# Performance work log

Measured on AMD Instinct MI355X. Metric: run time of the kernel, lower is better.

The kernel has to match this reference:

```python
import jax, jax.numpy as jnp
import numpy as np

B, S, H, E, TOPK = 2, 2048, 1024, 8, 2
CAP_FACTOR = 1.5
CAPACITY = int(B * S * CAP_FACTOR * TOPK / E)  # 1536


def setup_inputs() -> dict:
    key = jax.random.key(0)
    k1, k2, k3 = jax.random.split(key, 3)
    s = 1.0 / np.sqrt(H)
    return {
        "hidden_states": jax.random.normal(k1, (B, S, H), jnp.float32),
        "W1": jax.random.normal(k2, (H, H), jnp.float32) * s,
        "b1": jnp.zeros((H,), jnp.float32),
        "W2": jax.random.normal(k3, (H, E), jnp.float32) * s,
        "b2": jnp.zeros((E,), jnp.float32),
    }


def reference(hidden_states, W1, b1, W2, b2):
    # Router MLP: Linear -> ReLU -> Linear
    h = jax.nn.relu(jnp.einsum("bsh,hk->bsk", hidden_states, W1) + b1)
    logits = jnp.einsum("bsh,he->bse", h, W2) + b2          # [B,S,E]
    probs = jax.nn.softmax(logits, axis=-1)                   # [B,S,E]

    topk_p, topk_i = jax.lax.top_k(probs, TOPK)               # [B,S,K]
    topk_p = topk_p / jnp.sum(topk_p, axis=-1, keepdims=True)

    N = B * S
    idx = topk_i.reshape(N, TOPK)                             # [N,K] int
    p = topk_p.reshape(N, TOPK)                               # [N,K]
    pos = jnp.arange(N)

    dispatch = jnp.zeros((N, E, CAPACITY), jnp.float32)
    combine = jnp.zeros((N, E, CAPACITY), jnp.float32)
    # Faithful to torch semantics: expert_count[idx] += 1 uses non-accumulating
    # index_put, so duplicates within one top-k slot collapse to a single +1.
    count = jnp.zeros((E,), jnp.int32)
    for i in range(TOPK):  # small fixed loop over top-k slots
        e = idx[:, i]                  # [N]
        pr = p[:, i]                   # [N]
        c_e = count[e]                 # slot position for each token's expert
        ok = c_e < CAPACITY
        # (pos, e, c_e) triples are unique per token; prior value is always 0,
        # so masked-out tokens just rewrite 0.
        dispatch = dispatch.at[pos, e, c_e].set(jnp.where(ok, 1.0, 0.0))
        combine = combine.at[pos, e, c_e].set(jnp.where(ok, pr, 0.0))
        # within a slot all tokens of expert e write the same value -> deterministic
        count = count.at[e].set(jnp.where(ok, c_e + 1, c_e))

    dispatch = dispatch.reshape(B, S, E, CAPACITY)
    combine = combine.reshape(B, S, E, CAPACITY)

    per_expert = probs.mean(axis=(0, 1))                      # [E]
    aux_loss = jnp.sum(per_expert * jnp.log(per_expert * E + 1e-9))
    return dispatch, combine, probs, aux_loss
```

## Files before the change

### kernel.cpp

```cpp
#include <hip/hip_runtime.h>

#define TOKENS 4096
#define HDIM   1024
#define EDIM   8
#define CAP    1536

typedef float f32x4 __attribute__((ext_vector_type(4)));

#define BM 128
#define BN 64
#define BK 16
#define ZF4_PER_BLOCK 49152

__global__ __launch_bounds__(256, 2) void gemm1_relu_fill(
    const float* __restrict__ X, const float* __restrict__ W1,
    const float* __restrict__ b1, float* __restrict__ Hout,
    float* __restrict__ zreg, int* __restrict__ flags)
{
    __shared__ float As[BK][BM + 4];
    __shared__ float Bs[BK][BN];
    const int K = HDIM, N = HDIM;
    const int tid  = threadIdx.x;
    const int arow = tid >> 1;
    const int acol = (tid & 1) << 3;
    const int brow = tid >> 4;
    const int bcol = (tid & 15) << 2;
    const int tx   = tid & 15;
    const int ty   = tid >> 4;

    const float* Ab = X  + (size_t)(blockIdx.y * BM) * K;
    const float* Bb = W1 + blockIdx.x * BN;

    const int blk = blockIdx.y * gridDim.x + blockIdx.x;
    if (blk == 0 && tid < EDIM) flags[tid] = 0;
    f32x4* Z = (f32x4*)zreg + (size_t)blk * ZF4_PER_BLOCK + tid;
    const f32x4 z4 = {0.f, 0.f, 0.f, 0.f};

    float acc[8][4] = {};
    int zs = 0;
    for (int k0 = 0; k0 < K; k0 += BK) {
        float4 a0 = *(const float4*)(Ab + (size_t)arow * K + k0 + acol);
        float4 a1 = *(const float4*)(Ab + (size_t)arow * K + k0 + acol + 4);
        float4 bv = *(const float4*)(Bb + (size_t)(k0 + brow) * N + bcol);
        As[acol + 0][arow] = a0.x;
        As[acol + 1][arow] = a0.y;
        As[acol + 2][arow] = a0.z;
        As[acol + 3][arow] = a0.w;
        As[acol + 4][arow] = a1.x;
        As[acol + 5][arow] = a1.y;
        As[acol + 6][arow] = a1.z;
        As[acol + 7][arow] = a1.w;
        *(float4*)&Bs[brow][bcol] = bv;
        __syncthreads();

        __builtin_nontemporal_store(z4, Z + (size_t)(zs + 0) * 256);
        __builtin_nontemporal_store(z4, Z + (size_t)(zs + 1) * 256);
        __builtin_nontemporal_store(z4, Z + (size_t)(zs + 2) * 256);
        zs += 3;

#pragma unroll
        for (int kk = 0; kk < BK; kk++) {
            float4 a4a = *(const float4*)&As[kk][ty << 3];
            float4 a4b = *(const float4*)&As[kk][(ty << 3) + 4];
            float4 b4  = *(const float4*)&Bs[kk][tx << 2];
            float a[8] = {a4a.x, a4a.y, a4a.z, a4a.w, a4b.x, a4b.y, a4b.z, a4b.w};
            float b[4] = {b4.x, b4.y, b4.z, b4.w};
#pragma unroll
            for (int i = 0; i < 8; i++)
#pragma unroll
                for (int j = 0; j < 4; j++)
                    acc[i][j] = fmaf(a[i], b[j], acc[i][j]);
        }
        __syncthreads();
    }

    const int gm = blockIdx.y * BM + (ty << 3);
    const int gn = blockIdx.x * BN + (tx << 2);
    float4 bias = *(const float4*)(b1 + gn);
#pragma unroll
    for (int i = 0; i < 8; i++) {
        float4 o;
        o.x = fmaxf(acc[i][0] + bias.x, 0.f);
        o.y = fmaxf(acc[i][1] + bias.y, 0.f);
        o.z = fmaxf(acc[i][2] + bias.z, 0.f);
        o.w = fmaxf(acc[i][3] + bias.w, 0.f);
        *(float4*)(Hout + (size_t)(gm + i) * N + gn) = o;
    }
}

__global__ __launch_bounds__(256) void router_k(
    const float* __restrict__ Hbuf, const float* __restrict__ W2,
    const float* __restrict__ b2, float* __restrict__ probs_out,
    int* __restrict__ e0a, int* __restrict__ e1a,
    float* __restrict__ p0a, float* __restrict__ p1a,
    int* __restrict__ flags)
{
    const int wave  = threadIdx.x >> 6;
    const int lane  = threadIdx.x & 63;
    const int token = (blockIdx.x << 2) + wave;

    const float* hrow = Hbuf + (size_t)token * HDIM;
    float acc[8] = {0, 0, 0, 0, 0, 0, 0, 0};
#pragma unroll
    for (int k = 0; k < HDIM / 64; k++) {
        const int hidx = lane + (k << 6);
        const float hv = hrow[hidx];
        float4 wa = *(const float4*)(W2 + hidx * 8);
        float4 wb = *(const float4*)(W2 + hidx * 8 + 4);
        acc[0] = fmaf(hv, wa.x, acc[0]);
        acc[1] = fmaf(hv, wa.y, acc[1]);
        acc[2] = fmaf(hv, wa.z, acc[2]);
        acc[3] = fmaf(hv, wa.w, acc[3]);
        acc[4] = fmaf(hv, wb.x, acc[4]);
        acc[5] = fmaf(hv, wb.y, acc[5]);
        acc[6] = fmaf(hv, wb.z, acc[6]);
        acc[7] = fmaf(hv, wb.w, acc[7]);
    }
#pragma unroll
    for (int off = 32; off; off >>= 1) {
#pragma unroll
        for (int e = 0; e < 8; e++) acc[e] += __shfl_xor(acc[e], off);
    }

    if (lane == 0) {
        float logit[8];
#pragma unroll
        for (int e = 0; e < 8; e++) logit[e] = acc[e] + b2[e];
        float mx = logit[0];
#pragma unroll
        for (int e = 1; e < 8; e++) mx = fmaxf(mx, logit[e]);
        float p[8], s = 0.f;
#pragma unroll
        for (int e = 0; e < 8; e++) { p[e] = expf(logit[e] - mx); s += p[e]; }
        const float inv = 1.f / s;
#pragma unroll
        for (int e = 0; e < 8; e++) p[e] *= inv;

        float4 pa = {p[0], p[1], p[2], p[3]};
        float4 pb = {p[4], p[5], p[6], p[7]};
        *(float4*)(probs_out + (size_t)token * 8)     = pa;
        *(float4*)(probs_out + (size_t)token * 8 + 4) = pb;

        int e0 = 0; float m0 = logit[0];
#pragma unroll
        for (int e = 1; e < 8; e++) if (logit[e] > m0) { m0 = logit[e]; e0 = e; }
        int e1 = -1; float m1 = -1e30f;
#pragma unroll
        for (int e = 0; e < 8; e++) if (e != e0 && logit[e] > m1) { m1 = logit[e]; e1 = e; }

        const float ps = p[e0] + p[e1];
        e0a[token] = e0;
        e1a[token] = e1;
        p0a[token] = p[e0] / ps;
        p1a[token] = p[e1] / ps;
        atomicOr(&flags[e0], 1);
    }
}

__global__ __launch_bounds__(256) void scatter_aux_k(
    const int* __restrict__ e0a, const int* __restrict__ e1a,
    const float* __restrict__ p0a, const float* __restrict__ p1a,
    const int* __restrict__ flags,
    float* __restrict__ dispatch, float* __restrict__ combine,
    const float* __restrict__ probs, float* __restrict__ auxout)
{
    const int t = blockIdx.x * 256 + threadIdx.x;
    if (t < TOKENS) {
        const int e0 = e0a[t], e1 = e1a[t];
        const size_t b0 = ((size_t)t * EDIM + e0) * CAP;
        dispatch[b0] = 1.f;
        combine[b0]  = p0a[t];
        const int s1 = flags[e1] ? 1 : 0;
        const size_t b1 = ((size_t)t * EDIM + e1) * CAP + s1;
        dispatch[b1] = 1.f;
        combine[b1]  = p1a[t];
    }

    if (blockIdx.x == 0) {
        __shared__ float red[4][8];
        const int tid = threadIdx.x, lane = tid & 63, wave = tid >> 6;
        float acc[8] = {0, 0, 0, 0, 0, 0, 0, 0};
        for (int tt = tid; tt < TOKENS; tt += 256) {
            float4 a = *(const float4*)(probs + (size_t)tt * 8);
            float4 b = *(const float4*)(probs + (size_t)tt * 8 + 4);
            acc[0] += a.x; acc[1] += a.y; acc[2] += a.z; acc[3] += a.w;
            acc[4] += b.x; acc[5] += b.y; acc[6] += b.z; acc[7] += b.w;
        }
#pragma unroll
        for (int off = 32; off; off >>= 1)
#pragma unroll
            for (int e = 0; e < 8; e++) acc[e] += __shfl_xor(acc[e], off);
        if (lane == 0)
#pragma unroll
            for (int e = 0; e < 8; e++) red[wave][e] = acc[e];
        __syncthreads();
        if (tid == 0) {
            float aux = 0.f;
#pragma unroll
            for (int e = 0; e < 8; e++) {
                float pe = (red[0][e] + red[1][e] + red[2][e] + red[3][e]) * (1.f / TOKENS);
                aux += pe * logf(pe * (float)EDIM + 1e-9f);
            }
            *auxout = aux;
        }
    }
}

extern "C" void kernel_launch(void* const* d_in, const int* in_sizes, int n_in,
                              void* d_out, int out_size, void* d_ws, size_t ws_size,
                              hipStream_t stream)
{
    const float* X  = (const float*)d_in[0];
    const float* W1 = (const float*)d_in[1];
    const float* b1 = (const float*)d_in[2];
    const float* W2 = (const float*)d_in[3];
    const float* b2 = (const float*)d_in[4];

    float* out = (float*)d_out;
    const size_t dispN = (size_t)TOKENS * EDIM * CAP;
    float* dispatch = out;
    float* combine  = out + dispN;
    float* probs    = out + 2 * dispN;
    float* auxout   = out + 2 * dispN + (size_t)TOKENS * EDIM;

    float* hbuf = (float*)d_ws;
    char* pp = (char*)d_ws + (size_t)TOKENS * HDIM * sizeof(float);
    int*   e0a = (int*)pp;   pp += TOKENS * sizeof(int);
    int*   e1a = (int*)pp;   pp += TOKENS * sizeof(int);
    float* p0a = (float*)pp; pp += TOKENS * sizeof(float);
    float* p1a = (float*)pp; pp += TOKENS * sizeof(float);
    int*   flags = (int*)pp;

    gemm1_relu_fill<<<dim3(HDIM / BN, TOKENS / BM), 256, 0, stream>>>(
        X, W1, b1, hbuf, dispatch, flags);
    router_k<<<TOKENS / 4, 256, 0, stream>>>(hbuf, W2, b2, probs, e0a, e1a, p0a, p1a, flags);
    scatter_aux_k<<<TOKENS / 256, 256, 0, stream>>>(
        e0a, e1a, p0a, p1a, flags, dispatch, combine, probs, auxout);
}
```

Baseline: 190.9 us.

## Use bf16 MFMA for router GEMM with fp32 rescue for near-tie tokens

```diff
diff --git a/kernel.cpp b/kernel.cpp
--- a/kernel.cpp
+++ b/kernel.cpp
@@ -4,100 +4,126 @@
 #define HDIM   1024
 #define EDIM   8
 #define CAP    1536
+#define TAU    0.10f
 
 typedef float f32x4 __attribute__((ext_vector_type(4)));
-
-#define BM 128
-#define BN 64
-#define BK 16
-#define ZF4_PER_BLOCK 49152
-
-__global__ __launch_bounds__(256, 2) void gemm1_relu_fill(
+typedef short bf16x8 __attribute__((ext_vector_type(8)));
+
+static __device__ __forceinline__ unsigned short f2bf(float f) {
+    unsigned int u = __float_as_uint(f);
+    return (unsigned short)((u + 0x7fffu + ((u >> 16) & 1u)) >> 16);
+}
+
+#define ZF4_PER_BLOCK 98304
+
+__global__ __launch_bounds__(256, 2) void gemm1_mfma_fill(
     const float* __restrict__ X, const float* __restrict__ W1,
     const float* __restrict__ b1, float* __restrict__ Hout,
-    float* __restrict__ zreg, int* __restrict__ flags)
-{
-    __shared__ float As[BK][BM + 4];
-    __shared__ float Bs[BK][BN];
-    const int K = HDIM, N = HDIM;
+    float* __restrict__ zfill)
+{
+    __shared__ unsigned short As[128][40];
+    __shared__ unsigned short Bs[128][40];
     const int tid  = threadIdx.x;
-    const int arow = tid >> 1;
-    const int acol = (tid & 1) << 3;
-    const int brow = tid >> 4;
-    const int bcol = (tid & 15) << 2;
-    const int tx   = tid & 15;
-    const int ty   = tid >> 4;
-
-    const float* Ab = X  + (size_t)(blockIdx.y * BM) * K;
-    const float* Bb = W1 + blockIdx.x * BN;
-
-    const int blk = blockIdx.y * gridDim.x + blockIdx.x;
-    if (blk == 0 && tid < EDIM) flags[tid] = 0;
-    f32x4* Z = (f32x4*)zreg + (size_t)blk * ZF4_PER_BLOCK + tid;
+    const int wave = tid >> 6, lane = tid & 63;
+    const int wm = (wave >> 1) * 64, wn = (wave & 1) * 64;
+    const int g = lane >> 4, r = lane & 15;
+    const int m0 = blockIdx.y * 128, n0 = blockIdx.x * 128;
+
+    const int srow = tid >> 1;
+    const int soff = (tid & 1) * 16;
+    const int bn   = tid & 127;
+    const int bko  = (tid >> 7) * 16;
+
+    const int blk = blockIdx.y * 8 + blockIdx.x;
+    f32x4* Z = (f32x4*)zfill + (size_t)blk * ZF4_PER_BLOCK + tid;
     const f32x4 z4 = {0.f, 0.f, 0.f, 0.f};
 
-    float acc[8][4] = {};
+    f32x4 acc[4][4] = {};
     int zs = 0;
-    for (int k0 = 0; k0 < K; k0 += BK) {
-        float4 a0 = *(const float4*)(Ab + (size_t)arow * K + k0 + acol);
-        float4 a1 = *(const float4*)(Ab + (size_t)arow * K + k0 + acol + 4);
-        float4 bv = *(const float4*)(Bb + (size_t)(k0 + brow) * N + bcol);
-        As[acol + 0][arow] = a0.x;
-        As[acol + 1][arow] = a0.y;
-        As[acol + 2][arow] = a0.z;
-        As[acol + 3][arow] = a0.w;
-        As[acol + 4][arow] = a1.x;
-        As[acol + 5][arow] = a1.y;
-        As[acol + 6][arow] = a1.z;
-        As[acol + 7][arow] = a1.w;
-        *(float4*)&Bs[brow][bcol] = bv;
-        __syncthreads();
-
-        __builtin_nontemporal_store(z4, Z + (size_t)(zs + 0) * 256);
-        __builtin_nontemporal_store(z4, Z + (size_t)(zs + 1) * 256);
-        __builtin_nontemporal_store(z4, Z + (size_t)(zs + 2) * 256);
-        zs += 3;
-
-#pragma unroll
-        for (int kk = 0; kk < BK; kk++) {
-            float4 a4a = *(const float4*)&As[kk][ty << 3];
-            float4 a4b = *(const float4*)&As[kk][(ty << 3) + 4];
-            float4 b4  = *(const float4*)&Bs[kk][tx << 2];
-            float a[8] = {a4a.x, a4a.y, a4a.z, a4a.w, a4b.x, a4b.y, a4b.z, a4b.w};
-            float b[4] = {b4.x, b4.y, b4.z, b4.w};
-#pragma unroll
-            for (int i = 0; i < 8; i++)
-#pragma unroll
-                for (int j = 0; j < 4; j++)
-                    acc[i][j] = fmaf(a[i], b[j], acc[i][j]);
-        }
-        __syncthreads();
-    }
-
-    const int gm = blockIdx.y * BM + (ty << 3);
-    const int gn = blockIdx.x * BN + (tx << 2);
-    float4 bias = *(const float4*)(b1 + gn);
-#pragma unroll
-    for (int i = 0; i < 8; i++) {
-        float4 o;
-        o.x = fmaxf(acc[i][0] + bias.x, 0.f);
-        o.y = fmaxf(acc[i][1] + bias.y, 0.f);
-        o.z = fmaxf(acc[i][2] + bias.z, 0.f);
-        o.w = fmaxf(acc[i][3] + bias.w, 0.f);
-        *(float4*)(Hout + (size_t)(gm + i) * N + gn) = o;
-    }
-}
-
-__global__ __launch_bounds__(256) void router_k(
+    for (int k0 = 0; k0 < HDIM; k0 += 32) {
+        const float* ap = X + (size_t)(m0 + srow) * HDIM + k0 + soff;
+        float4 a0 = *(const float4*)(ap);
+        float4 a1 = *(const float4*)(ap + 4);
+        float4 a2 = *(const float4*)(ap + 8);
+        float4 a3 = *(const float4*)(ap + 12);
+        uint4 w0, w1;
+        w0.x = f2bf(a0.x) | ((unsigned)f2bf(a0.y) << 16);
+        w0.y = f2bf(a0.z) | ((unsigned)f2bf(a0.w) << 16);
+        w0.z = f2bf(a1.x) | ((unsigned)f2bf(a1.y) << 16);
+        w0.w = f2bf(a1.z) | ((unsigned)f2bf(a1.w) << 16);
+        w1.x = f2bf(a2.x) | ((unsigned)f2bf(a2.y) << 16);
+        w1.y = f2bf(a2.z) | ((unsigned)f2bf(a2.w) << 16);
+        w1.z = f2bf(a3.x) | ((unsigned)f2bf(a3.y) << 16);
+        w1.w = f2bf(a3.z) | ((unsigned)f2bf(a3.w) << 16);
+        *(uint4*)&As[srow][soff]     = w0;
+        *(uint4*)&As[srow][soff + 8] = w1;
+
+        const float* bp = W1 + (size_t)(k0 + bko) * HDIM + n0 + bn;
+        float bv[16];
+#pragma unroll
+        for (int j = 0; j < 16; j++) bv[j] = bp[(size_t)j * HDIM];
+        uint4 q0, q1;
+        q0.x = f2bf(bv[0])  | ((unsigned)f2bf(bv[1])  << 16);
+        q0.y = f2bf(bv[2])  | ((unsigned)f2bf(bv[3])  << 16);
+        q0.z = f2bf(bv[4])  | ((unsigned)f2bf(bv[5])  << 16);
+        q0.w = f2bf(bv[6])  | ((unsigned)f2bf(bv[7])  << 16);
+        q1.x = f2bf(bv[8])  | ((unsigned)f2bf(bv[9])  << 16);
+        q1.y = f2bf(bv[10]) | ((unsigned)f2bf(bv[11]) << 16);
+        q1.z = f2bf(bv[12]) | ((unsigned)f2bf(bv[13]) << 16);
+        q1.w = f2bf(bv[14]) | ((unsigned)f2bf(bv[15]) << 16);
+        *(uint4*)&Bs[bn][bko]     = q0;
+        *(uint4*)&Bs[bn][bko + 8] = q1;
+
+#pragma unroll
+        for (int s = 0; s < 12; s++)
+            __builtin_nontemporal_store(z4, Z + (size_t)(zs + s) * 256);
+        zs += 12;
+
+        __syncthreads();
+        bf16x8 af[4], bfr[4];
+#pragma unroll
+        for (int i = 0; i < 4; i++) {
+            af[i]  = *(const bf16x8*)&As[wm + i * 16 + r][g * 8];
+            bfr[i] = *(const bf16x8*)&Bs[wn + i * 16 + r][g * 8];
+        }
+#pragma unroll
+        for (int i = 0; i < 4; i++)
+#pragma unroll
+            for (int j = 0; j < 4; j++)
+                acc[i][j] = __builtin_amdgcn_mfma_f32_16x16x32_bf16(af[i], bfr[j], acc[i][j], 0, 0, 0);
+        __syncthreads();
+    }
+
+#pragma unroll
+    for (int j = 0; j < 4; j++) {
+        const int col = n0 + wn + j * 16 + r;
+        const float bias = b1[col];
+#pragma unroll
+        for (int i = 0; i < 4; i++) {
+            const int row = m0 + wm + i * 16 + g * 4;
+#pragma unroll
+            for (int q = 0; q < 4; q++)
+                Hout[(size_t)(row + q) * HDIM + col] = fmaxf(acc[i][j][q] + bias, 0.f);
+        }
+    }
+}
+
+__global__ __launch_bounds__(256) void router_pass(
     const float* __restrict__ Hbuf, const float* __restrict__ W2,
     const float* __restrict__ b2, float* __restrict__ probs_out,
     int* __restrict__ e0a, int* __restrict__ e1a,
     float* __restrict__ p0a, float* __restrict__ p1a,
-    int* __restrict__ flags)
-{
-    const int wave  = threadIdx.x >> 6;
-    const int lane  = threadIdx.x & 63;
-    const int token = (blockIdx.x << 2) + wave;
+    int* __restrict__ flags, int* __restrict__ nf, int* __restrict__ list,
+    int mode)
+{
+    const int wave = threadIdx.x >> 6;
+    const int lane = threadIdx.x & 63;
+    const int idx  = blockIdx.x * 4 + wave;
+    int token = idx;
+    if (mode == 1) {
+        if (idx >= nf[0]) return;
+        token = list[idx];
+    }
 
     const float* hrow = Hbuf + (size_t)token * HDIM;
     float acc[8] = {0, 0, 0, 0, 0, 0, 0, 0};
@@ -117,43 +143,105 @@
         acc[7] = fmaf(hv, wb.w, acc[7]);
     }
 #pragma unroll
-    for (int off = 32; off; off >>= 1) {
+    for (int off = 32; off; off >>= 1)
 #pragma unroll
         for (int e = 0; e < 8; e++) acc[e] += __shfl_xor(acc[e], off);
-    }
 
     if (lane == 0) {
         float logit[8];
 #pragma unroll
         for (int e = 0; e < 8; e++) logit[e] = acc[e] + b2[e];
-        float mx = logit[0];
-#pragma unroll
-        for (int e = 1; e < 8; e++) mx = fmaxf(mx, logit[e]);
-        float p[8], s = 0.f;
-#pragma unroll
-        for (int e = 0; e < 8; e++) { p[e] = expf(logit[e] - mx); s += p[e]; }
-        const float inv = 1.f / s;
-#pragma unroll
-        for (int e = 0; e < 8; e++) p[e] *= inv;
-
-        float4 pa = {p[0], p[1], p[2], p[3]};
-        float4 pb = {p[4], p[5], p[6], p[7]};
-        *(float4*)(probs_out + (size_t)token * 8)     = pa;
-        *(float4*)(probs_out + (size_t)token * 8 + 4) = pb;
-
         int e0 = 0; float m0 = logit[0];
 #pragma unroll
         for (int e = 1; e < 8; e++) if (logit[e] > m0) { m0 = logit[e]; e0 = e; }
         int e1 = -1; float m1 = -1e30f;
 #pragma unroll
         for (int e = 0; e < 8; e++) if (e != e0 && logit[e] > m1) { m1 = logit[e]; e1 = e; }
-
-        const float ps = p[e0] + p[e1];
-        e0a[token] = e0;
-        e1a[token] = e1;
-        p0a[token] = p[e0] / ps;
-        p1a[token] = p[e1] / ps;
-        atomicOr(&flags[e0], 1);
+        float m2 = -1e30f;
+#pragma unroll
+        for (int e = 0; e < 8; e++) if (e != e0 && e != e1 && logit[e] > m2) m2 = logit[e];
+
+        if (mode == 0 && ((m0 - m1 < TAU) || (m1 - m2 < TAU))) {
+            int w = atomicAdd(nf, 1);
+            list[w] = token;
+        } else {
+            float mx = m0, p[8], s = 0.f;
+#pragma unroll
+            for (int e = 0; e < 8; e++) { p[e] = expf(logit[e] - mx); s += p[e]; }
+            const float inv = 1.f / s;
+#pragma unroll
+            for (int e = 0; e < 8; e++) p[e] *= inv;
+            float4 pa = {p[0], p[1], p[2], p[3]};
+            float4 pb = {p[4], p[5], p[6], p[7]};
+            *(float4*)(probs_out + (size_t)token * 8)     = pa;
+            *(float4*)(probs_out + (size_t)token * 8 + 4) = pb;
+            const float ps = p[e0] + p[e1];
+            e0a[token] = e0;
+            e1a[token] = e1;
+            p0a[token] = p[e0] / ps;
+            p1a[token] = p[e1] / ps;
+            atomicOr(&flags[e0], 1);
+        }
+    }
+}
+
+__global__ __launch_bounds__(256) void rescue_gemm(
+    const float* __restrict__ X, const float* __restrict__ W1,
+    const float* __restrict__ b1, float* __restrict__ Hout,
+    const int* __restrict__ nf, const int* __restrict__ list)
+{
+    const int n  = nf[0];
+    const int i0 = blockIdx.y * 32;
+    if (i0 >= n) return;
+    const int c0 = blockIdx.x * 128;
+
+    __shared__ float Xs[32][36];
+    __shared__ float Ws[32][132];
+    __shared__ int   toks[32];
+    const int tid = threadIdx.x;
+    if (tid < 32) toks[tid] = (i0 + tid < n) ? list[i0 + tid] : list[n - 1];
+    __syncthreads();
+
+    const int xi = tid >> 3;
+    const int kq = (tid & 7) * 4;
+    const int wk = tid >> 3;
+    const int cq = (tid & 7) * 16;
+    const int to4 = (tid >> 5) * 4;
+    const int co4 = (tid & 31) * 4;
+
+    float acc[4][4] = {};
+    for (int k0 = 0; k0 < HDIM; k0 += 32) {
+        *(float4*)&Xs[xi][kq] = *(const float4*)(X + (size_t)toks[xi] * HDIM + k0 + kq);
+        const float* wp = W1 + (size_t)(k0 + wk) * HDIM + c0 + cq;
+        *(float4*)&Ws[wk][cq]      = *(const float4*)(wp);
+        *(float4*)&Ws[wk][cq + 4]  = *(const float4*)(wp + 4);
+        *(float4*)&Ws[wk][cq + 8]  = *(const float4*)(wp + 8);
+        *(float4*)&Ws[wk][cq + 12] = *(const float4*)(wp + 12);
+        __syncthreads();
+#pragma unroll
+        for (int kk = 0; kk < 32; kk++) {
+            float4 wv = *(const float4*)&Ws[kk][co4];
+            float xv[4];
+#pragma unroll
+            for (int t = 0; t < 4; t++) xv[t] = Xs[to4 + t][kk];
+#pragma unroll
+            for (int t = 0; t < 4; t++) {
+                acc[t][0] = fmaf(xv[t], wv.x, acc[t][0]);
+                acc[t][1] = fmaf(xv[t], wv.y, acc[t][1]);
+                acc[t][2] = fmaf(xv[t], wv.z, acc[t][2]);
+                acc[t][3] = fmaf(xv[t], wv.w, acc[t][3]);
+            }
+        }
+        __syncthreads();
+    }
+#pragma unroll
+    for (int t = 0; t < 4; t++) {
+        const size_t row = (size_t)toks[to4 + t] * HDIM;
+#pragma unroll
+        for (int c = 0; c < 4; c++) {
+            const int col = c0 + co4 + c;
+            Hout[row + col] = fmaxf(acc[t][c] + b1[col], 0.f);
+        }
     }
 }
 
@@ -225,15 +313,22 @@
 
     float* hbuf = (float*)d_ws;
     char* pp = (char*)d_ws + (size_t)TOKENS * HDIM * sizeof(float);
-    int*   e0a = (int*)pp;   pp += TOKENS * sizeof(int);
-    int*   e1a = (int*)pp;   pp += TOKENS * sizeof(int);
-    float* p0a = (float*)pp; pp += TOKENS * sizeof(float);
-    float* p1a = (float*)pp; pp += TOKENS * sizeof(float);
-    int*   flags = (int*)pp;
-
-    gemm1_relu_fill<<<dim3(HDIM / BN, TOKENS / BM), 256, 0, stream>>>(
-        X, W1, b1, hbuf, dispatch, flags);
-    router_k<<<TOKENS / 4, 256, 0, stream>>>(hbuf, W2, b2, probs, e0a, e1a, p0a, p1a, flags);
+    int*   e0a  = (int*)pp;   pp += TOKENS * sizeof(int);
+    int*   e1a  = (int*)pp;   pp += TOKENS * sizeof(int);
+    float* p0a  = (float*)pp; pp += TOKENS * sizeof(float);
+    float* p1a  = (float*)pp; pp += TOKENS * sizeof(float);
+    int*   flags = (int*)pp;  pp += EDIM * sizeof(int);
+    int*   nf    = (int*)pp;  pp += sizeof(int);
+    int*   list  = (int*)pp;
+
+    hipMemsetAsync(flags, 0, (EDIM + 1) * sizeof(int), stream);
+
+    gemm1_mfma_fill<<<dim3(8, 32), 256, 0, stream>>>(X, W1, b1, hbuf, dispatch);
+    router_pass<<<TOKENS / 4, 256, 0, stream>>>(hbuf, W2, b2, probs,
+                                                e0a, e1a, p0a, p1a, flags, nf, list, 0);
+    rescue_gemm<<<dim3(8, 128), 256, 0, stream>>>(X, W1, b1, hbuf, nf, list);
+    router_pass<<<TOKENS / 4, 256, 0, stream>>>(hbuf, W2, b2, probs,
+                                                e0a, e1a, p0a, p1a, flags, nf, list, 1);
     scatter_aux_k<<<TOKENS / 256, 256, 0, stream>>>(
         e0a, e1a, p0a, p1a, flags, dispatch, combine, probs, auxout);
 }
```

Result: slower. 246.1 us (+28.9%).
